# Kernel tuning notes

Measured on AMD Instinct MI355X. Metric: run time of the kernel, lower is better.

## Reference

```python
import jax, jax.numpy as jnp
import numpy as np

BL = 5           # block_len
BS = BL * BL     # block_size = 25
NH = 8           # num_heads
MASK_ONES = 12   # first 12 window positions unmasked (causal raster mask)


def _rel_pos_index():
    coords = np.stack(np.meshgrid(np.arange(BL), np.arange(BL), indexing='ij')).reshape(2, -1)
    rel = coords[:, :, None] - coords[:, None, :]          # [2, 25, 25]
    idx = (rel[0] + BL - 1) * (2 * BL - 1) + (rel[1] + BL - 1)
    return idx                                              # [25, 25] int

_REL_IDX = _rel_pos_index()


def _layernorm(x, w, b, eps=1e-5):
    m = jnp.mean(x, axis=-1, keepdims=True)
    v = jnp.var(x, axis=-1, keepdims=True)
    return (x - m) * jax.lax.rsqrt(v + eps) * w + b


def setup_inputs() -> dict:
    key = jax.random.key(0)
    ks = jax.random.split(key, 16)
    B, C, H, W = 4, 64, 64, 64
    out_dim = 64
    hidden = int(C * 4.0)
    s = lambda k, shape, scale=0.02: jax.random.normal(k, shape, dtype=jnp.float32) * scale
    return {
        'x': jax.random.normal(ks[0], (B, C, H, W), dtype=jnp.float32),
        'norm1_w': jnp.ones((C,), jnp.float32), 'norm1_b': jnp.zeros((C,), jnp.float32),
        'qkv_w': s(ks[1], (3 * C, C)), 'qkv_b': s(ks[2], (3 * C,)),
        'rpb_table': s(ks[3], ((2 * BL - 1) * (2 * BL - 1), NH)),
        'norm2_w': jnp.ones((C,), jnp.float32), 'norm2_b': jnp.zeros((C,), jnp.float32),
        'fc1_w': s(ks[4], (hidden, C)), 'fc1_b': s(ks[5], (hidden,)),
        'fc2_w': s(ks[6], (C, hidden)), 'fc2_b': s(ks[7], (C,)),
        'proj_w': s(ks[8], (out_dim, C)), 'proj_b': s(ks[9], (out_dim,)),
    }


def reference(x, norm1_w, norm1_b, qkv_w, qkv_b, rpb_table,
              norm2_w, norm2_b, fc1_w, fc1_b, fc2_w, fc2_b, proj_w, proj_b):
    B, C, H, W = x.shape
    hd = C // NH
    scale = hd ** (-0.5)

    # F.unfold(kernel=5, pad=2): per-pixel 5x5 neighborhood, channel-major then (kh,kw)
    xp = jnp.pad(x, ((0, 0), (0, 0), (2, 2), (2, 2)))
    patches = jnp.stack([xp[:, :, i:i + H, j:j + W] for i in range(BL) for j in range(BL)], axis=2)  # [B,C,25,H,W]
    x_unfold = patches.reshape(B, C, BS, H * W).transpose(0, 3, 2, 1)  # [B,HW,25,C]

    mask = (jnp.arange(BS) < MASK_ONES).astype(x.dtype)[None, None, :, None]
    x_masked = x_unfold * mask

    out = _layernorm(x_masked, norm1_w, norm1_b)
    qkv = out @ qkv_w.T + qkv_b                                 # [B,HW,25,3C]
    qkv = qkv.reshape(B, H * W, BS, 3, NH, hd).transpose(3, 0, 1, 4, 2, 5)  # [3,B,HW,nh,25,hd]
    q, k, v = qkv[0] * scale, qkv[1], qkv[2]

    attn = jnp.einsum('bpnqd,bpnkd->bpnqk', q, k)               # [B,HW,nh,25,25]
    bias = rpb_table[_REL_IDX.reshape(-1)].reshape(BS, BS, NH).transpose(2, 0, 1)  # [nh,25,25]
    attn = jax.nn.softmax(attn + bias[None, None], axis=-1)

    o = jnp.einsum('bpnqk,bpnkd->bpnqd', attn, v)               # [B,HW,nh,25,hd]
    o = o.transpose(0, 1, 3, 2, 4).reshape(B, H * W, BS, C)
    o = o + x_masked
    out_sumed = jnp.sum(o, axis=2)                              # [B,HW,C]

    y = _layernorm(out_sumed, norm2_w, norm2_b)
    y = jax.nn.gelu(y @ fc1_w.T + fc1_b, approximate=False) @ fc2_w.T + fc2_b
    y = y + out_sumed
    y = y @ proj_w.T + proj_b                                   # [B,HW,out_dim]
    return y.reshape(B, H, W, -1).transpose(0, 3, 1, 2)
```

## Files before the change

kernel.cpp:

```cpp
#include <hip/hip_runtime.h>
#include <hip/hip_bf16.h>


typedef _Float16 h2f __attribute__((ext_vector_type(2)));
typedef _Float16 h8  __attribute__((ext_vector_type(8)));
union u8h { h8 v; h2f p[4]; };

__device__ __forceinline__ float fdot2f(h2f a, h2f b, float c) {
#if defined(__has_builtin)
#if __has_builtin(__builtin_amdgcn_fdot2)
    return __builtin_amdgcn_fdot2(a, b, c, false);
#else
    return c + (float)a.x*(float)b.x + (float)a.y*(float)b.y;
#endif
#else
    return c + (float)a.x*(float)b.x + (float)a.y*(float)b.y;
#endif
}
__device__ __forceinline__ float dot8(u8h a, u8h b) {
    float c = 0.f;
    c = fdot2f(a.p[0], b.p[0], c);
    c = fdot2f(a.p[1], b.p[1], c);
    c = fdot2f(a.p[2], b.p[2], c);
    c = fdot2f(a.p[3], b.p[3], c);
    return c;
}
__device__ __forceinline__ float frcp(float x) {
#if defined(__has_builtin)
#if __has_builtin(__builtin_amdgcn_rcpf)
    return __builtin_amdgcn_rcpf(x);
#else
    return 1.0f/x;
#endif
#else
    return 1.0f/x;
#endif
}

#define SC 0.35355339059327373f

__global__ __launch_bounds__(256, 4) void k_qkv(
    const float* __restrict__ x, const float* __restrict__ n1w, const float* __restrict__ n1b,
    const float* __restrict__ qw, const float* __restrict__ qb, const float* __restrict__ rpb,
    const float* __restrict__ w1, const float* __restrict__ w2, const float* __restrict__ pw,
    _Float16* __restrict__ qkv, _Float16* __restrict__ qkvc_h,
    _Float16* __restrict__ ebh, float* __restrict__ ebs,
    _Float16* __restrict__ w1h, _Float16* __restrict__ w2h, _Float16* __restrict__ pwh,
    float* __restrict__ osT)
{
    const int t = threadIdx.x;
    const int bid = blockIdx.x;
    if (bid >= 512) {
        if (bid == 768) {
            if (t < 192) {
                float acc = qb[t];
                for (int c = 0; c < 64; ++c) acc += n1b[c]*qw[t*64 + c];
                qkvc_h[t] = (_Float16)acc;
            }
            for (int i = t; i < 2400; i += 256) {
                int h = i/300, r = i%300, q = r/12, k = r%12;
                int idx = (q/5 - k/5 + 4)*9 + (q%5 - k%5 + 4);
                ebh[i] = (_Float16)__expf(rpb[idx*8 + h]);
            }
            for (int i = t; i < 200; i += 256) {
                int h = i/25, q = i%25; float s = 0.f;
                for (int k = 12; k < 25; ++k) {
                    int idx = (q/5 - k/5 + 4)*9 + (q%5 - k%5 + 4);
                    s += __expf(rpb[idx*8 + h]);
                }
                ebs[i] = s;
            }
            for (int i = t; i < 16384; i += 256) w1h[i] = (_Float16)w1[i];
            for (int i = t; i < 16384; i += 256) w2h[i] = (_Float16)w2[i];
            for (int i = t; i < 4096;  i += 256) pwh[i] = (_Float16)pw[i];
            return;
        }
        for (int i = 0; i < 16; ++i) {
            int idx = (bid - 512)*4096 + i*256 + t;
            int c = idx >> 14, p = idx & 16383, b = p >> 12, hw = p & 4095;
            int hh = hw >> 6, ww = hw & 63;
            const float* pl = x + b*262144 + c*4096;
            float s = 0.f;
            #pragma unroll
            for (int dr = -2; dr <= 0; ++dr) {
                int r = hh + dr; if (r < 0) continue;
                int cmax = (dr == 0) ? -1 : 2;
                #pragma unroll
                for (int dc = -2; dc <= 2; ++dc) {
                    if (dc > cmax) break;
                    int w2c = ww + dc;
                    if (w2c >= 0 && w2c < 64) s += pl[(r << 6) + w2c];
                }
            }
            osT[(size_t)c*16384 + p] = s;
        }
        return;
    }
    __shared__ alignas(16) h2f sw[6144];
    __shared__ float sX[2080];
    __shared__ alignas(16) _Float16 sOut[6400];
    for (int i = t; i < 6144; i += 256) {
        float2 v = *(const float2*)(qw + i*2);
        sw[i] = h2f{(_Float16)v.x, (_Float16)v.y};
    }
    const int p0 = bid*32;
    const int b = p0 >> 12, hw0 = p0 & 4095;
    for (int i = t; i < 2048; i += 256) {
        int c = i >> 5, pp = i & 31;
        sX[pp*65 + c] = x[b*262144 + c*4096 + hw0 + pp];
    }
    __syncthreads();
    const int pix = t & 31, g = t >> 5;
    float s = 0.f, s2 = 0.f;
    #pragma unroll
    for (int c = 0; c < 64; ++c) { float v = sX[pix*65 + c]; s += v; s2 += v*v; }
    float m = s*0.015625f;
    float rstd = rsqrtf(fmaxf(s2*0.015625f - m*m, 0.f) + 1e-5f);
    h2f av[32];
    #pragma unroll
    for (int c = 0; c < 32; ++c) {
        float e0 = (sX[pix*65 + 2*c]     - m)*rstd*n1w[2*c]     + n1b[2*c];
        float e1 = (sX[pix*65 + 2*c + 1] - m)*rstd*n1w[2*c + 1] + n1b[2*c + 1];
        av[c] = h2f{(_Float16)e0, (_Float16)e1};
    }
    for (int i = 0; i < 24; ++i) {
        int o = g*24 + i;
        const h2f* wr = sw + o*32;
        float acc = qb[o];
        #pragma unroll
        for (int cp = 0; cp < 32; ++cp) acc = fdot2f(av[cp], wr[cp], acc);
        sOut[pix*200 + o] = (_Float16)acc;
    }
    __syncthreads();
    for (int i = t; i < 768; i += 256) {
        int pp = i/24, d4 = i%24;
        ((float4*)qkv)[(size_t)p0*24 + i] = *(const float4*)(sOut + pp*200 + d4*8);
    }
}

__global__ __launch_bounds__(512, 4) void k_attn(
    const _Float16* __restrict__ qkv, const _Float16* __restrict__ qkvc_h,
    const _Float16* __restrict__ ebh, const float* __restrict__ ebs,
    float* __restrict__ osT)
{
    __shared__ alignas(16) _Float16 sq[21600];
    __shared__ _Float16 seb[2400];
    __shared__ float sebs[200];
    __shared__ alignas(16) _Float16 sqc[192];
    __shared__ float red[6656];
    const int t = threadIdx.x;
    const int p0 = blockIdx.x*32;
    const int b = p0 >> 12, hw0 = p0 & 4095, hrow = hw0 >> 6, w0 = hw0 & 63;

    for (int i = t; i < 1200; i += 512) ((float*)seb)[i] = ((const float*)ebh)[i];
    for (int i = t; i < 200; i += 512) sebs[i] = ebs[i];
    if (t < 96) ((float*)sqc)[t] = ((const float*)qkvc_h)[t];
    for (int i = t; i < 2592; i += 512) {
        int row = i/24, d4 = i%24;
        int rr = row/36, cc = row%36;
        int gr = hrow - 2 + rr, gc = w0 - 2 + cc;
        float4 v;
        if (gr >= 0 && gc >= 0 && gc < 64)
            v = ((const float4*)qkv)[(size_t)((b << 12) + (gr << 6) + gc)*24 + d4];
        else
            v = ((const float4*)qkvc_h)[d4];
        *(float4*)(sq + row*200 + d4*8) = v;
    }
    __syncthreads();

    const int pix = t & 31, h = (t >> 5) & 7, half = t >> 8, hb = h*8;
    u8h kreg[12];
    #pragma unroll
    for (int k = 0; k < 12; ++k) {
        int rw = (k/5)*36 + pix + (k%5);
        kreg[k].v = *(const h8*)(sq + rw*200 + 64 + hb);
    }
    u8h kc; kc.v = *(const h8*)(sqc + 64 + hb);

    float w[13];
    #pragma unroll
    for (int k = 0; k < 13; ++k) w[k] = 0.f;

    const int qlo = half ? 9 : 0, qhi = half ? 12 : 9;
    for (int sIdx = qlo; sIdx < qhi; ++sIdx) {
        int rw = (sIdx/5)*36 + pix + (sIdx%5);
        u8h qu; qu.v = *(const h8*)(sq + rw*200 + hb);
        const _Float16* ebr = seb + (h*25 + sIdx)*12;
        float rs = __expf(dot8(qu, kc)*SC) * sebs[h*25 + sIdx];
        float wcq = rs;
        float tt[12];
        #pragma unroll
        for (int k = 0; k < 12; ++k) {
            float e = __expf(dot8(qu, kreg[k])*SC) * (float)ebr[k];
            tt[k] = e; rs += e;
        }
        float inv = frcp(rs);
        #pragma unroll
        for (int k = 0; k < 12; ++k) w[k] += tt[k]*inv;
        w[12] += wcq*inv;
    }
    if (half) {
        u8h qcu; qcu.v = *(const h8*)(sqc + hb);
        float edc[12];
        #pragma unroll
        for (int k = 0; k < 12; ++k) edc[k] = __expf(dot8(qcu, kreg[k])*SC);
        float ecc = __expf(dot8(qcu, kc)*SC);
        for (int q = 12; q < 25; ++q) {
            const _Float16* ebr = seb + (h*25 + q)*12;
            float rs = ecc * sebs[h*25 + q];
            float wcq = rs;
            float tt[12];
            #pragma unroll
            for (int k = 0; k < 12; ++k) { float e = edc[k]*(float)ebr[k]; tt[k] = e; rs += e; }
            float inv = frcp(rs);
            #pragma unroll
            for (int k = 0; k < 12; ++k) w[k] += tt[k]*inv;
            w[12] += wcq*inv;
        }
    }
    const int ph = (h << 5) + pix;
    {
        float* my = red + (ph*2 + half)*13;
        #pragma unroll
        for (int k = 0; k < 13; ++k) my[k] = w[k];
    }
    __syncthreads();
    {
        const float* ot = red + (ph*2 + (half ^ 1))*13;
        #pragma unroll
        for (int k = 0; k < 13; ++k) w[k] += ot[k];
    }
    const int d0 = half*4;
    float out0, out1, out2, out3;
    {
        const h2f* vcp = (const h2f*)(sqc + 128 + hb + d0);
        h2f v0 = vcp[0], v1 = vcp[1];
        out0 = w[12]*(float)v0.x; out1 = w[12]*(float)v0.y;
        out2 = w[12]*(float)v1.x; out3 = w[12]*(float)v1.y;
    }
    #pragma unroll
    for (int k = 0; k < 12; ++k) {
        int rw = (k/5)*36 + pix + (k%5);
        const h2f* vp = (const h2f*)(sq + rw*200 + 128 + hb + d0);
        h2f v0 = vp[0], v1 = vp[1];
        float wk = w[k];
        out0 += wk*(float)v0.x; out1 += wk*(float)v0.y;
        out2 += wk*(float)v1.x; out3 += wk*(float)v1.y;
    }
    const int p = p0 + pix;
    float* op = osT + (size_t)(hb + d0)*16384 + p;
    op[0]       += out0;
    op[16384]   += out1;
    op[32768]   += out2;
    op[49152]   += out3;
}

__global__ __launch_bounds__(512, 4) void k_mlp(
    const float* __restrict__ osT, const float* __restrict__ n2w, const float* __restrict__ n2b,
    const float* __restrict__ b1, const float* __restrict__ b2, const float* __restrict__ pb,
    const _Float16* __restrict__ w1h, const _Float16* __restrict__ w2h, const _Float16* __restrict__ pwh,
    float* __restrict__ out)
{
    __shared__ float sA[2112];
    __shared__ h2f sAv[1088];
    __shared__ alignas(16) _Float16 sH[8448];
    __shared__ alignas(16) _Float16 sY[2304];
    __shared__ float sb1[256], sb2[64], spb[64], sM[32], sR[32], sN[128];
    const int t = threadIdx.x;
    const int p0 = blockIdx.x*32;
    for (int i = t; i < 2048; i += 512) {
        int c = i >> 5, pp = i & 31;
        sA[pp*66 + c] = osT[(size_t)c*16384 + p0 + pp];
    }
    if (t < 256) sb1[t] = b1[t];
    else if (t < 320) sb2[t - 256] = b2[t - 256];
    else if (t < 384) spb[t - 320] = pb[t - 320];
    else if (t < 448) sN[t - 384] = n2w[t - 384];
    else sN[64 + (t - 448)] = n2b[t - 448];
    __syncthreads();
    if (t < 32) {
        float s = 0.f, s2 = 0.f;
        for (int c = 0; c < 64; ++c) { float v = sA[t*66 + c]; s += v; s2 += v*v; }
        float m = s*0.015625f;
        sM[t] = m; sR[t] = rsqrtf(fmaxf(s2*0.015625f - m*m, 0.f) + 1e-5f);
    }
    __syncthreads();
    for (int i = t; i < 1024; i += 512) {
        int pp = i >> 5, pr = i & 31;
        float m = sM[pp], r = sR[pp];
        float e0 = (sA[pp*66 + 2*pr]     - m)*r*sN[2*pr]     + sN[64 + 2*pr];
        float e1 = (sA[pp*66 + 2*pr + 1] - m)*r*sN[2*pr + 1] + sN[64 + 2*pr + 1];
        sAv[pp*34 + pr] = h2f{(_Float16)e0, (_Float16)e1};
    }
    __syncthreads();
    const int pix = t & 31, sl = t >> 5;
    const int p = p0 + pix;
    const h2f* avr = sAv + pix*34;
    for (int i = 0; i < 16; ++i) {
        int j = sl*16 + i;
        const h2f* wr = (const h2f*)(w1h + j*64);
        float acc = sb1[j];
        #pragma unroll
        for (int cp = 0; cp < 32; ++cp) acc = fdot2f(avr[cp], wr[cp], acc);
        float g = 0.5f*acc*(1.f + erff(acc*0.70710678118654752f));
        sH[pix*264 + j] = (_Float16)g;
    }
    __syncthreads();
    const h2f* hr = (const h2f*)(sH + pix*264);
    for (int mm = 0; mm < 4; ++mm) {
        int o = sl*4 + mm;
        const h2f* wr = (const h2f*)(w2h + o*256);
        float acc = sb2[o];
        #pragma unroll 32
        for (int jp = 0; jp < 128; ++jp) acc = fdot2f(hr[jp], wr[jp], acc);
        float y = acc + osT[(size_t)o*16384 + p];
        sY[pix*72 + o] = (_Float16)y;
    }
    __syncthreads();
    const int bimg = p >> 12, hw = p & 4095, hh = hw >> 6, ww = hw & 63;
    const h2f* yr = (const h2f*)(sY + pix*72);
    for (int mm = 0; mm < 4; ++mm) {
        int o = sl*4 + mm;
        const h2f* wr = (const h2f*)(pwh + o*64);
        float acc = spb[o];
        #pragma unroll
        for (int c = 0; c < 32; ++c) acc = fdot2f(yr[c], wr[c], acc);
        out[(size_t)(((bimg*64 + o)*64 + hh)*64) + ww] = acc;
    }
}

extern "C" void kernel_launch(void* const* d_in, const int* in_sizes, int n_in,
                              void* d_out, int out_size, void* d_ws, size_t ws_size,
                              hipStream_t stream) {
    const float* x   = (const float*)d_in[0];
    const float* n1w = (const float*)d_in[1];
    const float* n1b = (const float*)d_in[2];
    const float* qw  = (const float*)d_in[3];
    const float* qb  = (const float*)d_in[4];
    const float* rpb = (const float*)d_in[5];
    const float* n2w = (const float*)d_in[6];
    const float* n2b = (const float*)d_in[7];
    const float* w1  = (const float*)d_in[8];
    const float* b1  = (const float*)d_in[9];
    const float* w2  = (const float*)d_in[10];
    const float* b2  = (const float*)d_in[11];
    const float* pw  = (const float*)d_in[12];
    const float* pb  = (const float*)d_in[13];
    float* out = (float*)d_out;

    float* ws = (float*)d_ws;
    _Float16* qkv    = (_Float16*)ws;
    float*    osT    = ws + 1572864;
    _Float16* qkvc_h = (_Float16*)(ws + 2621440);
    _Float16* ebh    = (_Float16*)(ws + 2621536);
    float*    ebsp   = ws + 2622736;
    _Float16* w1h    = (_Float16*)(ws + 2622936);
    _Float16* w2h    = (_Float16*)(ws + 2631128);
    _Float16* pwh    = (_Float16*)(ws + 2639320);

    hipLaunchKernelGGL(k_qkv, dim3(769), dim3(256), 0, stream,
                       x, n1w, n1b, qw, qb, rpb, w1, w2, pw,
                       qkv, qkvc_h, ebh, ebsp, w1h, w2h, pwh, osT);
    hipLaunchKernelGGL(k_attn, dim3(512), dim3(512), 0, stream,
                       qkv, qkvc_h, ebh, ebsp, osT);
    hipLaunchKernelGGL(k_mlp, dim3(512), dim3(512), 0, stream,
                       osT, n2w, n2b, b1, b2, pb, w1h, w2h, pwh, out);
}
```

Baseline: 190.3 us.

## Restructure all three kernels with new thread mappings and register-resident rows

All three kernels are rewritten. The QKV kernel now keeps each pixel's 64 channels in registers, does fp32 FMA against global weights four outputs at a time, and computes the window-sum residual from a padded shared-memory plane. Attention now splits the 12 keys between two half-warps that combine results with shuffles, uses 16-pixel tiles with a smaller halo, and packs the bias table into 8-wide rows. The MLP kernel keeps LayerNorm inputs in registers and computes four outputs per thread with 64-pixel blocks, writing coalesced output rows. The intent is less shared-memory traffic and fewer barriers, at the cost of higher register pressure and a changed occupancy.

```diff
diff --git a/kernel.cpp b/kernel.cpp
--- a/kernel.cpp
+++ b/kernel.cpp
@@ -5,6 +5,7 @@
 typedef _Float16 h2f __attribute__((ext_vector_type(2)));
 typedef _Float16 h8  __attribute__((ext_vector_type(8)));
 union u8h { h8 v; h2f p[4]; };
+union pk4 { _Float16 h[4]; unsigned int u[2]; };
 
 __device__ __forceinline__ float fdot2f(h2f a, h2f b, float c) {
 #if defined(__has_builtin)
@@ -39,293 +40,279 @@
 
 #define SC 0.35355339059327373f
 
-__global__ __launch_bounds__(256, 4) void k_qkv(
+__global__ __launch_bounds__(1024) void k_qkv(
     const float* __restrict__ x, const float* __restrict__ n1w, const float* __restrict__ n1b,
     const float* __restrict__ qw, const float* __restrict__ qb, const float* __restrict__ rpb,
     const float* __restrict__ w1, const float* __restrict__ w2, const float* __restrict__ pw,
-    _Float16* __restrict__ qkv, _Float16* __restrict__ qkvc_h,
-    _Float16* __restrict__ ebh, float* __restrict__ ebs,
+    _Float16* __restrict__ qkvh, _Float16* __restrict__ qkvc_h, _Float16* __restrict__ eb7,
     _Float16* __restrict__ w1h, _Float16* __restrict__ w2h, _Float16* __restrict__ pwh,
     float* __restrict__ osT)
 {
+    __shared__ float sxp[68*68];
+    const int t = threadIdx.x, bid = blockIdx.x;
+    if (bid < 256) {
+        const int pix = t & 63, g = t >> 6;
+        const int p = bid*64 + pix;
+        const int b = p >> 12, hw = p & 4095;
+        const float* xp = x + (size_t)b*262144 + hw;
+        float xr[64]; float s = 0.f, s2 = 0.f;
+        #pragma unroll
+        for (int c = 0; c < 64; ++c) { float v = xp[(size_t)c*4096]; xr[c] = v; s += v; s2 += v*v; }
+        float m = s*0.015625f;
+        float rstd = rsqrtf(fmaxf(s2*0.015625f - m*m, 0.f) + 1e-5f);
+        #pragma unroll
+        for (int c = 0; c < 64; ++c) xr[c] = (xr[c] - m)*rstd*n1w[c] + n1b[c];
+        _Float16* orow = qkvh + (size_t)p*192;
+        #pragma unroll
+        for (int i4 = 0; i4 < 12; i4 += 4) {
+            const int o = g*12 + i4;
+            const float* wr = qw + o*64;
+            float a0 = qb[o], a1 = qb[o+1], a2 = qb[o+2], a3 = qb[o+3];
+            #pragma unroll 16
+            for (int c = 0; c < 64; ++c) {
+                float xv = xr[c];
+                a0 += xv*wr[c]; a1 += xv*wr[64+c]; a2 += xv*wr[128+c]; a3 += xv*wr[192+c];
+            }
+            pk4 pk;
+            pk.h[0]=(_Float16)a0; pk.h[1]=(_Float16)a1; pk.h[2]=(_Float16)a2; pk.h[3]=(_Float16)a3;
+            *(uint2*)(orow + o) = make_uint2(pk.u[0], pk.u[1]);
+        }
+        return;
+    }
+    if (bid < 512) {
+        const int plane = bid - 256;
+        for (int i = t; i < 4624; i += 1024) sxp[i] = 0.f;
+        __syncthreads();
+        const float* xp = x + (size_t)plane*4096;
+        for (int i = t; i < 4096; i += 1024) {
+            int r = i >> 6, w = i & 63;
+            sxp[(r + 2)*68 + (w + 2)] = xp[i];
+        }
+        __syncthreads();
+        const int c = plane & 63, b = plane >> 6;
+        float* op = osT + (size_t)c*16384 + b*4096;
+        for (int i = t; i < 4096; i += 1024) {
+            int r = i >> 6, w = i & 63;
+            const float* s0 = sxp + r*68 + w;
+            float sv = s0[0]+s0[1]+s0[2]+s0[3]+s0[4]
+                     + s0[68]+s0[69]+s0[70]+s0[71]+s0[72]
+                     + s0[136]+s0[137];
+            op[i] = sv;
+        }
+        return;
+    }
+    if (bid < 520) {
+        const int cid = bid - 512;
+        for (int i = t; i < 4608; i += 1024) {
+            int j = cid*4608 + i;
+            if (j < 16384)      w1h[j]          = (_Float16)w1[j];
+            else if (j < 32768) w2h[j - 16384]  = (_Float16)w2[j - 16384];
+            else                pwh[j - 32768]  = (_Float16)pw[j - 32768];
+        }
+        return;
+    }
+    if (t < 192) {
+        float acc = qb[t];
+        for (int c = 0; c < 64; ++c) acc += n1b[c]*qw[t*64 + c];
+        qkvc_h[t] = (_Float16)acc;
+    }
+    for (int i = t; i < 3200; i += 1024) {
+        int j = i & 7, hf = (i >> 3) & 1, r = i >> 4;
+        int h = r/25, q = r - h*25;
+        float v = 0.f;
+        if (j < 6) {
+            int k = hf*6 + j;
+            int ridx = (q/5 - k/5 + 4)*9 + (q%5 - k%5 + 4);
+            v = __expf(rpb[ridx*8 + h]);
+        } else if (j == 6 && hf) {
+            for (int k = 12; k < 25; ++k) {
+                int ridx = (q/5 - k/5 + 4)*9 + (q%5 - k%5 + 4);
+                v += __expf(rpb[ridx*8 + h]);
+            }
+        }
+        eb7[i] = (_Float16)v;
+    }
+}
+
+__global__ __launch_bounds__(256) void k_attn(
+    const _Float16* __restrict__ qkvh, const _Float16* __restrict__ qkvc_h,
+    const _Float16* __restrict__ eb7g, float* __restrict__ osT)
+{
+    __shared__ alignas(16) _Float16 sq[60*200];
+    __shared__ alignas(16) _Float16 seb[3200];
+    __shared__ alignas(16) _Float16 sqc[192];
     const int t = threadIdx.x;
-    const int bid = blockIdx.x;
-    if (bid >= 512) {
-        if (bid == 768) {
-            if (t < 192) {
-                float acc = qb[t];
-                for (int c = 0; c < 64; ++c) acc += n1b[c]*qw[t*64 + c];
-                qkvc_h[t] = (_Float16)acc;
-            }
-            for (int i = t; i < 2400; i += 256) {
-                int h = i/300, r = i%300, q = r/12, k = r%12;
-                int idx = (q/5 - k/5 + 4)*9 + (q%5 - k%5 + 4);
-                ebh[i] = (_Float16)__expf(rpb[idx*8 + h]);
-            }
-            for (int i = t; i < 200; i += 256) {
-                int h = i/25, q = i%25; float s = 0.f;
-                for (int k = 12; k < 25; ++k) {
-                    int idx = (q/5 - k/5 + 4)*9 + (q%5 - k%5 + 4);
-                    s += __expf(rpb[idx*8 + h]);
-                }
-                ebs[i] = s;
-            }
-            for (int i = t; i < 16384; i += 256) w1h[i] = (_Float16)w1[i];
-            for (int i = t; i < 16384; i += 256) w2h[i] = (_Float16)w2[i];
-            for (int i = t; i < 4096;  i += 256) pwh[i] = (_Float16)pw[i];
-            return;
-        }
-        for (int i = 0; i < 16; ++i) {
-            int idx = (bid - 512)*4096 + i*256 + t;
-            int c = idx >> 14, p = idx & 16383, b = p >> 12, hw = p & 4095;
-            int hh = hw >> 6, ww = hw & 63;
-            const float* pl = x + b*262144 + c*4096;
-            float s = 0.f;
-            #pragma unroll
-            for (int dr = -2; dr <= 0; ++dr) {
-                int r = hh + dr; if (r < 0) continue;
-                int cmax = (dr == 0) ? -1 : 2;
-                #pragma unroll
-                for (int dc = -2; dc <= 2; ++dc) {
-                    if (dc > cmax) break;
-                    int w2c = ww + dc;
-                    if (w2c >= 0 && w2c < 64) s += pl[(r << 6) + w2c];
-                }
-            }
-            osT[(size_t)c*16384 + p] = s;
-        }
-        return;
-    }
-    __shared__ alignas(16) h2f sw[6144];
-    __shared__ float sX[2080];
-    __shared__ alignas(16) _Float16 sOut[6400];
-    for (int i = t; i < 6144; i += 256) {
-        float2 v = *(const float2*)(qw + i*2);
-        sw[i] = h2f{(_Float16)v.x, (_Float16)v.y};
-    }
-    const int p0 = bid*32;
-    const int b = p0 >> 12, hw0 = p0 & 4095;
-    for (int i = t; i < 2048; i += 256) {
-        int c = i >> 5, pp = i & 31;
-        sX[pp*65 + c] = x[b*262144 + c*4096 + hw0 + pp];
+    const int p0 = blockIdx.x*16;
+    const int b = p0 >> 12, hw0 = p0 & 4095, hrow = hw0 >> 6, w0c = hw0 & 63;
+
+    for (int i = t; i < 1600; i += 256) ((unsigned int*)seb)[i] = ((const unsigned int*)eb7g)[i];
+    if (t < 96) ((unsigned int*)sqc)[t] = ((const unsigned int*)qkvc_h)[t];
+    for (int i = t; i < 1440; i += 256) {
+        int row = i/24, d4 = i%24;
+        int rr = row/20, cc = row%20;
+        int gr = hrow - 2 + rr, gc = w0c - 2 + cc;
+        float4 v = (gr >= 0 && gc >= 0 && gc < 64)
+            ? ((const float4*)qkvh)[(size_t)((b << 12) + (gr << 6) + gc)*24 + d4]
+            : ((const float4*)qkvc_h)[d4];
+        *(float4*)(sq + row*200 + d4*8) = v;
     }
     __syncthreads();
-    const int pix = t & 31, g = t >> 5;
-    float s = 0.f, s2 = 0.f;
-    #pragma unroll
-    for (int c = 0; c < 64; ++c) { float v = sX[pix*65 + c]; s += v; s2 += v*v; }
-    float m = s*0.015625f;
-    float rstd = rsqrtf(fmaxf(s2*0.015625f - m*m, 0.f) + 1e-5f);
-    h2f av[32];
-    #pragma unroll
-    for (int c = 0; c < 32; ++c) {
-        float e0 = (sX[pix*65 + 2*c]     - m)*rstd*n1w[2*c]     + n1b[2*c];
-        float e1 = (sX[pix*65 + 2*c + 1] - m)*rstd*n1w[2*c + 1] + n1b[2*c + 1];
-        av[c] = h2f{(_Float16)e0, (_Float16)e1};
-    }
-    for (int i = 0; i < 24; ++i) {
-        int o = g*24 + i;
-        const h2f* wr = sw + o*32;
-        float acc = qb[o];
-        #pragma unroll
-        for (int cp = 0; cp < 32; ++cp) acc = fdot2f(av[cp], wr[cp], acc);
-        sOut[pix*200 + o] = (_Float16)acc;
-    }
-    __syncthreads();
-    for (int i = t; i < 768; i += 256) {
-        int pp = i/24, d4 = i%24;
-        ((float4*)qkv)[(size_t)p0*24 + i] = *(const float4*)(sOut + pp*200 + d4*8);
-    }
-}
-
-__global__ __launch_bounds__(512, 4) void k_attn(
-    const _Float16* __restrict__ qkv, const _Float16* __restrict__ qkvc_h,
-    const _Float16* __restrict__ ebh, const float* __restrict__ ebs,
-    float* __restrict__ osT)
-{
-    __shared__ alignas(16) _Float16 sq[21600];
-    __shared__ _Float16 seb[2400];
-    __shared__ float sebs[200];
-    __shared__ alignas(16) _Float16 sqc[192];
-    __shared__ float red[6656];
-    const int t = threadIdx.x;
-    const int p0 = blockIdx.x*32;
-    const int b = p0 >> 12, hw0 = p0 & 4095, hrow = hw0 >> 6, w0 = hw0 & 63;
-
-    for (int i = t; i < 1200; i += 512) ((float*)seb)[i] = ((const float*)ebh)[i];
-    for (int i = t; i < 200; i += 512) sebs[i] = ebs[i];
-    if (t < 96) ((float*)sqc)[t] = ((const float*)qkvc_h)[t];
-    for (int i = t; i < 2592; i += 512) {
-        int row = i/24, d4 = i%24;
-        int rr = row/36, cc = row%36;
-        int gr = hrow - 2 + rr, gc = w0 - 2 + cc;
-        float4 v;
-        if (gr >= 0 && gc >= 0 && gc < 64)
-            v = ((const float4*)qkv)[(size_t)((b << 12) + (gr << 6) + gc)*24 + d4];
-        else
-            v = ((const float4*)qkvc_h)[d4];
-        *(float4*)(sq + row*200 + d4*8) = v;
-    }
-    __syncthreads();
-
-    const int pix = t & 31, h = (t >> 5) & 7, half = t >> 8, hb = h*8;
-    u8h kreg[12];
-    #pragma unroll
-    for (int k = 0; k < 12; ++k) {
-        int rw = (k/5)*36 + pix + (k%5);
-        kreg[k].v = *(const h8*)(sq + rw*200 + 64 + hb);
-    }
-    u8h kc; kc.v = *(const h8*)(sqc + 64 + hb);
-
-    float w[13];
-    #pragma unroll
-    for (int k = 0; k < 13; ++k) w[k] = 0.f;
-
-    const int qlo = half ? 9 : 0, qhi = half ? 12 : 9;
-    for (int sIdx = qlo; sIdx < qhi; ++sIdx) {
-        int rw = (sIdx/5)*36 + pix + (sIdx%5);
-        u8h qu; qu.v = *(const h8*)(sq + rw*200 + hb);
-        const _Float16* ebr = seb + (h*25 + sIdx)*12;
-        float rs = __expf(dot8(qu, kc)*SC) * sebs[h*25 + sIdx];
-        float wcq = rs;
-        float tt[12];
-        #pragma unroll
-        for (int k = 0; k < 12; ++k) {
-            float e = __expf(dot8(qu, kreg[k])*SC) * (float)ebr[k];
-            tt[k] = e; rs += e;
-        }
+
+    const int pix = t & 15, hf = (t >> 4) & 1, h = t >> 5, hb = h*8;
+    int rws[6];
+    #pragma unroll
+    for (int j = 0; j < 6; ++j) { int k = hf*6 + j; rws[j] = (k/5)*20 + pix + (k%5); }
+    u8h kreg[7];
+    #pragma unroll
+    for (int j = 0; j < 6; ++j) kreg[j].v = *(const h8*)(sq + rws[j]*200 + 64 + hb);
+    kreg[6].v = hf ? *(const h8*)(sqc + 64 + hb) : kreg[0].v;
+    u8h qcu; qcu.v = *(const h8*)(sqc + hb);
+    float edc[7];
+    #pragma unroll
+    for (int j = 0; j < 7; ++j) edc[j] = __expf(dot8(qcu, kreg[j])*SC);
+    float w[7];
+    #pragma unroll
+    for (int j = 0; j < 7; ++j) w[j] = 0.f;
+    const _Float16* ebbase = seb + h*400 + hf*8;
+
+    for (int sIdx = 0; sIdx < 12; ++sIdx) {
+        int rq = (sIdx/5)*20 + pix + (sIdx%5);
+        u8h qu; qu.v = *(const h8*)(sq + rq*200 + hb);
+        h8 eb8 = *(const h8*)(ebbase + sIdx*16);
+        float e[7]; float rs = 0.f;
+        #pragma unroll
+        for (int j = 0; j < 7; ++j) {
+            float ev = __expf(dot8(qu, kreg[j])*SC)*(float)eb8[j];
+            e[j] = ev; rs += ev;
+        }
+        rs += __shfl_xor(rs, 16);
         float inv = frcp(rs);
         #pragma unroll
-        for (int k = 0; k < 12; ++k) w[k] += tt[k]*inv;
-        w[12] += wcq*inv;
-    }
-    if (half) {
-        u8h qcu; qcu.v = *(const h8*)(sqc + hb);
-        float edc[12];
-        #pragma unroll
-        for (int k = 0; k < 12; ++k) edc[k] = __expf(dot8(qcu, kreg[k])*SC);
-        float ecc = __expf(dot8(qcu, kc)*SC);
-        for (int q = 12; q < 25; ++q) {
-            const _Float16* ebr = seb + (h*25 + q)*12;
-            float rs = ecc * sebs[h*25 + q];
-            float wcq = rs;
-            float tt[12];
-            #pragma unroll
-            for (int k = 0; k < 12; ++k) { float e = edc[k]*(float)ebr[k]; tt[k] = e; rs += e; }
-            float inv = frcp(rs);
-            #pragma unroll
-            for (int k = 0; k < 12; ++k) w[k] += tt[k]*inv;
-            w[12] += wcq*inv;
-        }
-    }
-    const int ph = (h << 5) + pix;
-    {
-        float* my = red + (ph*2 + half)*13;
-        #pragma unroll
-        for (int k = 0; k < 13; ++k) my[k] = w[k];
-    }
-    __syncthreads();
-    {
-        const float* ot = red + (ph*2 + (half ^ 1))*13;
-        #pragma unroll
-        for (int k = 0; k < 13; ++k) w[k] += ot[k];
-    }
-    const int d0 = half*4;
-    float out0, out1, out2, out3;
-    {
-        const h2f* vcp = (const h2f*)(sqc + 128 + hb + d0);
-        h2f v0 = vcp[0], v1 = vcp[1];
-        out0 = w[12]*(float)v0.x; out1 = w[12]*(float)v0.y;
-        out2 = w[12]*(float)v1.x; out3 = w[12]*(float)v1.y;
-    }
-    #pragma unroll
-    for (int k = 0; k < 12; ++k) {
-        int rw = (k/5)*36 + pix + (k%5);
-        const h2f* vp = (const h2f*)(sq + rw*200 + 128 + hb + d0);
-        h2f v0 = vp[0], v1 = vp[1];
-        float wk = w[k];
-        out0 += wk*(float)v0.x; out1 += wk*(float)v0.y;
-        out2 += wk*(float)v1.x; out3 += wk*(float)v1.y;
-    }
-    const int p = p0 + pix;
-    float* op = osT + (size_t)(hb + d0)*16384 + p;
-    op[0]       += out0;
-    op[16384]   += out1;
-    op[32768]   += out2;
-    op[49152]   += out3;
-}
-
-__global__ __launch_bounds__(512, 4) void k_mlp(
+        for (int j = 0; j < 7; ++j) w[j] += e[j]*inv;
+    }
+    for (int q = 12; q < 25; ++q) {
+        h8 eb8 = *(const h8*)(ebbase + q*16);
+        float e[7]; float rs = 0.f;
+        #pragma unroll
+        for (int j = 0; j < 7; ++j) {
+            float ev = edc[j]*(float)eb8[j];
+            e[j] = ev; rs += ev;
+        }
+        rs += __shfl_xor(rs, 16);
+        float inv = frcp(rs);
+        #pragma unroll
+        for (int j = 0; j < 7; ++j) w[j] += e[j]*inv;
+    }
+    float out[8];
+    #pragma unroll
+    for (int d = 0; d < 8; ++d) out[d] = 0.f;
+    #pragma unroll
+    for (int j = 0; j < 7; ++j) {
+        const _Float16* vp = (j < 6) ? (sq + rws[j]*200 + 128 + hb)
+                                     : (hf ? sqc + 128 + hb : sq + rws[0]*200 + 128 + hb);
+        u8h vv; vv.v = *(const h8*)vp;
+        float wj = w[j];
+        #pragma unroll
+        for (int d4 = 0; d4 < 4; ++d4) {
+            h2f pr = vv.p[d4];
+            out[d4*2]   += wj*(float)pr.x;
+            out[d4*2+1] += wj*(float)pr.y;
+        }
+    }
+    #pragma unroll
+    for (int d = 0; d < 8; ++d) out[d] += __shfl_xor(out[d], 16);
+    const int p = p0 + pix, dbase = hf*4;
+    float* op = osT + (size_t)(hb + dbase)*16384 + p;
+    op[0]     += out[dbase];
+    op[16384] += out[dbase + 1];
+    op[32768] += out[dbase + 2];
+    op[49152] += out[dbase + 3];
+}
+
+__global__ __launch_bounds__(1024) void k_mlp(
     const float* __restrict__ osT, const float* __restrict__ n2w, const float* __restrict__ n2b,
     const float* __restrict__ b1, const float* __restrict__ b2, const float* __restrict__ pb,
     const _Float16* __restrict__ w1h, const _Float16* __restrict__ w2h, const _Float16* __restrict__ pwh,
     float* __restrict__ out)
 {
-    __shared__ float sA[2112];
-    __shared__ h2f sAv[1088];
-    __shared__ alignas(16) _Float16 sH[8448];
-    __shared__ alignas(16) _Float16 sY[2304];
-    __shared__ float sb1[256], sb2[64], spb[64], sM[32], sR[32], sN[128];
+    __shared__ alignas(16) _Float16 sH[64*258];
+    __shared__ alignas(16) _Float16 sY[64*74];
     const int t = threadIdx.x;
-    const int p0 = blockIdx.x*32;
-    for (int i = t; i < 2048; i += 512) {
-        int c = i >> 5, pp = i & 31;
-        sA[pp*66 + c] = osT[(size_t)c*16384 + p0 + pp];
-    }
-    if (t < 256) sb1[t] = b1[t];
-    else if (t < 320) sb2[t - 256] = b2[t - 256];
-    else if (t < 384) spb[t - 320] = pb[t - 320];
-    else if (t < 448) sN[t - 384] = n2w[t - 384];
-    else sN[64 + (t - 448)] = n2b[t - 448];
+    const int pix = t & 63, g = t >> 6;
+    const int p = blockIdx.x*64 + pix;
+    float a[64]; float s = 0.f, s2 = 0.f;
+    #pragma unroll
+    for (int c = 0; c < 64; ++c) { float v = osT[(size_t)c*16384 + p]; a[c] = v; s += v; s2 += v*v; }
+    float m = s*0.015625f;
+    float rstd = rsqrtf(fmaxf(s2*0.015625f - m*m, 0.f) + 1e-5f);
+    h2f av[32];
+    #pragma unroll
+    for (int c = 0; c < 32; ++c) {
+        float e0 = (a[2*c]   - m)*rstd*n2w[2*c]   + n2b[2*c];
+        float e1 = (a[2*c+1] - m)*rstd*n2w[2*c+1] + n2b[2*c+1];
+        av[c] = h2f{(_Float16)e0, (_Float16)e1};
+    }
+    #pragma unroll
+    for (int i4 = 0; i4 < 16; i4 += 4) {
+        const int j = g*16 + i4;
+        const h2f* wr = (const h2f*)(w1h + (size_t)j*64);
+        float a0 = b1[j], a1 = b1[j+1], a2 = b1[j+2], a3 = b1[j+3];
+        #pragma unroll
+        for (int cp = 0; cp < 32; ++cp) {
+            h2f xv = av[cp];
+            a0 = fdot2f(xv, wr[cp],      a0);
+            a1 = fdot2f(xv, wr[32 + cp], a1);
+            a2 = fdot2f(xv, wr[64 + cp], a2);
+            a3 = fdot2f(xv, wr[96 + cp], a3);
+        }
+        sH[pix*258 + j]     = (_Float16)(0.5f*a0*(1.f + erff(a0*0.70710678f)));
+        sH[pix*258 + j + 1] = (_Float16)(0.5f*a1*(1.f + erff(a1*0.70710678f)));
+        sH[pix*258 + j + 2] = (_Float16)(0.5f*a2*(1.f + erff(a2*0.70710678f)));
+        sH[pix*258 + j + 3] = (_Float16)(0.5f*a3*(1.f + erff(a3*0.70710678f)));
+    }
     __syncthreads();
-    if (t < 32) {
-        float s = 0.f, s2 = 0.f;
-        for (int c = 0; c < 64; ++c) { float v = sA[t*66 + c]; s += v; s2 += v*v; }
-        float m = s*0.015625f;
-        sM[t] = m; sR[t] = rsqrtf(fmaxf(s2*0.015625f - m*m, 0.f) + 1e-5f);
+    {
+        const int o = g*4;
+        const h2f* wr = (const h2f*)(w2h + (size_t)o*256);
+        const h2f* hr = (const h2f*)(sH + pix*258);
+        float a0 = b2[o], a1 = b2[o+1], a2 = b2[o+2], a3 = b2[o+3];
+        #pragma unroll 32
+        for (int jp = 0; jp < 128; ++jp) {
+            h2f hv = hr[jp];
+            a0 = fdot2f(hv, wr[jp],       a0);
+            a1 = fdot2f(hv, wr[128 + jp], a1);
+            a2 = fdot2f(hv, wr[256 + jp], a2);
+            a3 = fdot2f(hv, wr[384 + jp], a3);
+        }
+        a0 += osT[(size_t)o*16384 + p];
+        a1 += osT[(size_t)(o+1)*16384 + p];
+        a2 += osT[(size_t)(o+2)*16384 + p];
+        a3 += osT[(size_t)(o+3)*16384 + p];
+        sY[pix*74 + o]     = (_Float16)a0;
+        sY[pix*74 + o + 1] = (_Float16)a1;
+        sY[pix*74 + o + 2] = (_Float16)a2;
+        sY[pix*74 + o + 3] = (_Float16)a3;
     }
     __syncthreads();
-    for (int i = t; i < 1024; i += 512) {
-        int pp = i >> 5, pr = i & 31;
-        float m = sM[pp], r = sR[pp];
-        float e0 = (sA[pp*66 + 2*pr]     - m)*r*sN[2*pr]     + sN[64 + 2*pr];
-        float e1 = (sA[pp*66 + 2*pr + 1] - m)*r*sN[2*pr + 1] + sN[64 + 2*pr + 1];
-        sAv[pp*34 + pr] = h2f{(_Float16)e0, (_Float16)e1};
-    }
-    __syncthreads();
-    const int pix = t & 31, sl = t >> 5;
-    const int p = p0 + pix;
-    const h2f* avr = sAv + pix*34;
-    for (int i = 0; i < 16; ++i) {
-        int j = sl*16 + i;
-        const h2f* wr = (const h2f*)(w1h + j*64);
-        float acc = sb1[j];
-        #pragma unroll
-        for (int cp = 0; cp < 32; ++cp) acc = fdot2f(avr[cp], wr[cp], acc);
-        float g = 0.5f*acc*(1.f + erff(acc*0.70710678118654752f));
-        sH[pix*264 + j] = (_Float16)g;
-    }
-    __syncthreads();
-    const h2f* hr = (const h2f*)(sH + pix*264);
-    for (int mm = 0; mm < 4; ++mm) {
-        int o = sl*4 + mm;
-        const h2f* wr = (const h2f*)(w2h + o*256);
-        float acc = sb2[o];
-        #pragma unroll 32
-        for (int jp = 0; jp < 128; ++jp) acc = fdot2f(hr[jp], wr[jp], acc);
-        float y = acc + osT[(size_t)o*16384 + p];
-        sY[pix*72 + o] = (_Float16)y;
-    }
-    __syncthreads();
-    const int bimg = p >> 12, hw = p & 4095, hh = hw >> 6, ww = hw & 63;
-    const h2f* yr = (const h2f*)(sY + pix*72);
-    for (int mm = 0; mm < 4; ++mm) {
-        int o = sl*4 + mm;
-        const h2f* wr = (const h2f*)(pwh + o*64);
-        float acc = spb[o];
-        #pragma unroll
-        for (int c = 0; c < 32; ++c) acc = fdot2f(yr[c], wr[c], acc);
-        out[(size_t)(((bimg*64 + o)*64 + hh)*64) + ww] = acc;
+    {
+        const int o = g*4;
+        const h2f* wr = (const h2f*)(pwh + (size_t)o*64);
+        const h2f* yr = (const h2f*)(sY + pix*74);
+        float a0 = pb[o], a1 = pb[o+1], a2 = pb[o+2], a3 = pb[o+3];
+        #pragma unroll
+        for (int cp = 0; cp < 32; ++cp) {
+            h2f yv = yr[cp];
+            a0 = fdot2f(yv, wr[cp],      a0);
+            a1 = fdot2f(yv, wr[32 + cp], a1);
+            a2 = fdot2f(yv, wr[64 + cp], a2);
+            a3 = fdot2f(yv, wr[96 + cp], a3);
+        }
+        const int bimg = blockIdx.x >> 6, hh = blockIdx.x & 63;
+        float* ob = out + ((size_t)((bimg*64 + o)*64 + hh))*64 + pix;
+        ob[0]     = a0;
+        ob[4096]  = a1;
+        ob[8192]  = a2;
+        ob[12288] = a3;
     }
 }
 
@@ -349,20 +336,19 @@
     float* out = (float*)d_out;
 
     float* ws = (float*)d_ws;
-    _Float16* qkv    = (_Float16*)ws;
+    _Float16* qkvh   = (_Float16*)ws;
     float*    osT    = ws + 1572864;
     _Float16* qkvc_h = (_Float16*)(ws + 2621440);
-    _Float16* ebh    = (_Float16*)(ws + 2621536);
-    float*    ebsp   = ws + 2622736;
-    _Float16* w1h    = (_Float16*)(ws + 2622936);
-    _Float16* w2h    = (_Float16*)(ws + 2631128);
-    _Float16* pwh    = (_Float16*)(ws + 2639320);
-
-    hipLaunchKernelGGL(k_qkv, dim3(769), dim3(256), 0, stream,
+    _Float16* eb7    = (_Float16*)(ws + 2621536);
+    _Float16* w1h    = (_Float16*)(ws + 2623136);
+    _Float16* w2h    = (_Float16*)(ws + 2631328);
+    _Float16* pwh    = (_Float16*)(ws + 2639520);
+
+    hipLaunchKernelGGL(k_qkv, dim3(521), dim3(1024), 0, stream,
                        x, n1w, n1b, qw, qb, rpb, w1, w2, pw,
-                       qkv, qkvc_h, ebh, ebsp, w1h, w2h, pwh, osT);
-    hipLaunchKernelGGL(k_attn, dim3(512), dim3(512), 0, stream,
-                       qkv, qkvc_h, ebh, ebsp, osT);
-    hipLaunchKernelGGL(k_mlp, dim3(512), dim3(512), 0, stream,
+                       qkvh, qkvc_h, eb7, w1h, w2h, pwh, osT);
+    hipLaunchKernelGGL(k_attn, dim3(1024), dim3(256), 0, stream,
+                       qkvh, qkvc_h, eb7, osT);
+    hipLaunchKernelGGL(k_mlp, dim3(256), dim3(1024), 0, stream,
                        osT, n2w, n2b, b1, b2, pb, w1h, w2h, pwh, out);
 }
```

Result: slower. 239.4 us (+25.8%).
